# Kernel optimization log

Hardware: AMD Instinct MI355X
Metric: run time of the kernel (lower is better)

Reference implementation:

```python
import jax, jax.numpy as jnp
import numpy as np

N = 50000   # nodes
E = 800000  # edges (avg degree 16)
IN = 3      # in_feats = value(1) + u(2)
H = 128     # hid_feats


def setup_inputs() -> dict:
    key = jax.random.key(0)
    ks = jax.random.split(key, 24)
    value = jax.random.normal(ks[0], (N, 1), jnp.float32)
    u = jax.random.normal(ks[1], (N, 2), jnp.float32)
    src = jax.random.randint(ks[2], (E,), 0, N, dtype=jnp.int32)
    dst = jax.random.randint(ks[3], (E,), 0, N, dtype=jnp.int32)
    dims = [IN, H // 2, H, H, H, H, H, H, H, H, 1]
    inp = {"value": value, "u": u, "src": src, "dst": dst}
    for i in range(10):
        inp[f"W{i+1}"] = jax.random.normal(ks[4 + i], (dims[i], dims[i + 1]), jnp.float32) / np.sqrt(dims[i]).astype(np.float32)
        inp[f"b{i+1}"] = jnp.zeros((dims[i + 1],), jnp.float32)
    return inp


def _gconv(x, src, dst, inv_deg, W, b):
    # DGL GraphConv norm='right': sum incoming src features, divide by in-degree, linear, bias
    agg = jax.ops.segment_sum(x[src], dst, num_segments=N)  # [N, d_in]
    return (agg * inv_deg) @ W + b


def reference(value, u, src, dst, W1, b1, W2, b2, W3, b3, W4, b4, W5, b5,
              W6, b6, W7, b7, W8, b8, W9, b9, W10, b10):
    deg = jax.ops.segment_sum(jnp.ones((E,), jnp.float32), dst, num_segments=N)
    inv_deg = (1.0 / jnp.clip(deg, 1.0))[:, None]  # DGL clamps in-degree to >=1
    lrelu = lambda h: jax.nn.leaky_relu(h, 0.01)
    x = jnp.concatenate([value, u], axis=1)  # [N, 3]
    h = _gconv(x, src, dst, inv_deg, W1, b1)
    h = lrelu(_gconv(h, src, dst, inv_deg, W2, b2))
    h = lrelu(_gconv(h, src, dst, inv_deg, W3, b3))
    h = lrelu(_gconv(h, src, dst, inv_deg, W4, b4))
    h = _gconv(h, src, dst, inv_deg, W5, b5)
    h = _gconv(h, src, dst, inv_deg, W6, b6)
    h = _gconv(h, src, dst, inv_deg, W7, b7)
    h = _gconv(h, src, dst, inv_deg, W8, b8)
    h = jax.nn.sigmoid(_gconv(h, src, dst, inv_deg, W9, b9))
    h = _gconv(h, src, dst, inv_deg, W10, b10)  # [N, 1]
    return h
```

## Files before the change

kernel.cpp:

```cpp
#include <hip/hip_runtime.h>
#include <math.h>

typedef unsigned int u32;
typedef unsigned short u16;
using bf16x8 = __attribute__((ext_vector_type(8))) short;
using f32x4 = __attribute__((ext_vector_type(4))) float;

__device__ inline float bf_lo(u32 v) { return __uint_as_float(v << 16); }
__device__ inline float bf_hi(u32 v) { return __uint_as_float(v & 0xFFFF0000u); }
__device__ inline u16 f2bf(float f) {
    u32 u = __float_as_uint(f);
    return (u16)((u + 0x7FFFu + ((u >> 16) & 1u)) >> 16);
}
__device__ inline float bf2f(u16 h) { return __uint_as_float((u32)h << 16); }
__device__ inline float invdeg(int d) { return 1.0f / (float)(d > 1 ? d : 1); }

#define BIN_SHIFT 13

struct W7 { const float* p[7]; };

__global__ __launch_bounds__(256) void k_front(const int* __restrict__ src,
                                               const int* __restrict__ dst,
                                               int* __restrict__ cur,
                                               u16* __restrict__ colp,
                                               int E, int EB, int SB,
                                               const float* __restrict__ value,
                                               const float* __restrict__ u,
                                               float4* __restrict__ x4, int n, int NBx4,
                                               W7 wp, const float* __restrict__ W64,
                                               u16* __restrict__ hi128, u16* __restrict__ lo128,
                                               u16* __restrict__ hi64, u16* __restrict__ lo64) {
    int blk = blockIdx.x;
    if (blk < SB) {
        const int bin = blk / EB;
        int e = (blk - bin * EB) * 256 + threadIdx.x;
        if (e >= E) return;
        int d = dst[e];
        if ((d >> BIN_SHIFT) != bin) return;
        int slot = atomicAdd(&cur[d], 1);
        if (slot < 64) colp[(size_t)d * 64 + slot] = (u16)src[e];
        return;
    }
    int pb = blk - SB;
    if (pb < NBx4) {
        int i = pb * 256 + threadIdx.x;
        if (i < n) x4[i] = make_float4(value[i], u[2 * i], u[2 * i + 1], 0.f);
        return;
    }
    pb -= NBx4;
    if (pb < 56) {
        const int l = pb >> 3;
        const float* W = wp.p[l];
        int g = (pb & 7) * 256 + threadIdx.x;
        int ct = g >> 8;
        int rem = g & 255;
        int ks = rem >> 6;
        int lane = rem & 63;
        int kbase = ks * 32 + ((lane >> 4) << 3);
        int nn = (ct << 4) + (lane & 15);
        size_t off = ((size_t)l * 2048 + g) * 8;
#pragma unroll
        for (int j = 0; j < 8; ++j) {
            float w = W[(size_t)(kbase + j) * 128 + nn];
            u16 h = f2bf(w);
            hi128[off + j] = h;
            lo128[off + j] = f2bf(w - bf2f(h));
        }
    } else {
        int g = (pb - 56) * 256 + threadIdx.x;
        int ct = g >> 7;
        int rem = g & 127;
        int ks = rem >> 6;
        int lane = rem & 63;
        int kbase = ks * 32 + ((lane >> 4) << 3);
        int nn = (ct << 4) + (lane & 15);
        size_t off = (size_t)g * 8;
#pragma unroll
        for (int j = 0; j < 8; ++j) {
            float w = W64[(size_t)(kbase + j) * 128 + nn];
            u16 h = f2bf(w);
            hi64[off + j] = h;
            lo64[off + j] = f2bf(w - bf2f(h));
        }
    }
}

__global__ __launch_bounds__(256) void k_l1(const float4* __restrict__ x4,
                                            const u16* __restrict__ colp,
                                            const int* __restrict__ deg,
                                            const float* __restrict__ W1,
                                            const float* __restrict__ b1,
                                            u16* __restrict__ out, int nNodes) {
    const int lane = threadIdx.x & 63;
    const int n = blockIdx.x * 4 + (threadIdx.x >> 6);
    if (n >= nNodes) return;
    int dfull = deg[n];
    int dg = dfull > 64 ? 64 : dfull;
    const u16* cl = colp + (size_t)n * 64;
    float a0 = 0.f, a1 = 0.f, a2 = 0.f;
    if (lane < dg) {
        float4 v = x4[cl[lane]];
        a0 = v.x; a1 = v.y; a2 = v.z;
    }
#pragma unroll
    for (int o = 32; o; o >>= 1) {
        a0 += __shfl_xor(a0, o, 64);
        a1 += __shfl_xor(a1, o, 64);
        a2 += __shfl_xor(a2, o, 64);
    }
    float iv = invdeg(dfull);
    float y = b1[lane] + iv * (a0 * W1[lane] + a1 * W1[64 + lane] + a2 * W1[128 + lane]);
    out[(size_t)n * 64 + lane] = f2bf(y);
}

template <int ACT>
__device__ inline float actf(float x) {
    if (ACT == 1) return x > 0.f ? x : 0.01f * x;
    if (ACT == 2) return 1.f / (1.f + expf(-x));
    return x;
}

template <int DIN>
__device__ inline void agg_node(const void* __restrict__ Hin, const u16* __restrict__ colp,
                                const int* __restrict__ deg, u16* __restrict__ aggbuf,
                                int n, int lane) {
    int dfull = deg[n];
    int dg = dfull > 64 ? 64 : dfull;
    const u16* cl = colp + (size_t)n * 64;
    int myc = (lane < dg) ? (int)cl[lane] : 0;
    if (DIN == 128) {
        const u32* H32 = (const u32*)Hin;
        float a0 = 0.f, a1 = 0.f, b0 = 0.f, b1 = 0.f;
        int j = 0;
        for (; j + 8 <= dg; j += 8) {
            u32 v0 = H32[(size_t)__builtin_amdgcn_readlane(myc, j + 0) * 64 + lane];
            u32 v1 = H32[(size_t)__builtin_amdgcn_readlane(myc, j + 1) * 64 + lane];
            u32 v2 = H32[(size_t)__builtin_amdgcn_readlane(myc, j + 2) * 64 + lane];
            u32 v3 = H32[(size_t)__builtin_amdgcn_readlane(myc, j + 3) * 64 + lane];
            u32 v4 = H32[(size_t)__builtin_amdgcn_readlane(myc, j + 4) * 64 + lane];
            u32 v5 = H32[(size_t)__builtin_amdgcn_readlane(myc, j + 5) * 64 + lane];
            u32 v6 = H32[(size_t)__builtin_amdgcn_readlane(myc, j + 6) * 64 + lane];
            u32 v7 = H32[(size_t)__builtin_amdgcn_readlane(myc, j + 7) * 64 + lane];
            a0 += bf_lo(v0) + bf_lo(v1) + bf_lo(v2) + bf_lo(v3);
            a1 += bf_hi(v0) + bf_hi(v1) + bf_hi(v2) + bf_hi(v3);
            b0 += bf_lo(v4) + bf_lo(v5) + bf_lo(v6) + bf_lo(v7);
            b1 += bf_hi(v4) + bf_hi(v5) + bf_hi(v6) + bf_hi(v7);
        }
        for (; j + 4 <= dg; j += 4) {
            u32 v0 = H32[(size_t)__builtin_amdgcn_readlane(myc, j + 0) * 64 + lane];
            u32 v1 = H32[(size_t)__builtin_amdgcn_readlane(myc, j + 1) * 64 + lane];
            u32 v2 = H32[(size_t)__builtin_amdgcn_readlane(myc, j + 2) * 64 + lane];
            u32 v3 = H32[(size_t)__builtin_amdgcn_readlane(myc, j + 3) * 64 + lane];
            a0 += bf_lo(v0) + bf_lo(v1);
            a1 += bf_hi(v0) + bf_hi(v1);
            b0 += bf_lo(v2) + bf_lo(v3);
            b1 += bf_hi(v2) + bf_hi(v3);
        }
        for (; j < dg; ++j) {
            u32 v = H32[(size_t)__builtin_amdgcn_readlane(myc, j) * 64 + lane];
            a0 += bf_lo(v);
            a1 += bf_hi(v);
        }
        float iv = invdeg(dfull);
        ((u32*)aggbuf)[(size_t)n * 64 + lane] =
            (u32)f2bf((a0 + b0) * iv) | ((u32)f2bf((a1 + b1) * iv) << 16);
    } else {
        const u16* H16 = (const u16*)Hin;
        float a0 = 0.f, a1 = 0.f, b0 = 0.f, b1 = 0.f;
        int j = 0;
        for (; j + 8 <= dg; j += 8) {
            u16 v0 = H16[(size_t)__builtin_amdgcn_readlane(myc, j + 0) * 64 + lane];
            u16 v1 = H16[(size_t)__builtin_amdgcn_readlane(myc, j + 1) * 64 + lane];
            u16 v2 = H16[(size_t)__builtin_amdgcn_readlane(myc, j + 2) * 64 + lane];
            u16 v3 = H16[(size_t)__builtin_amdgcn_readlane(myc, j + 3) * 64 + lane];
            u16 v4 = H16[(size_t)__builtin_amdgcn_readlane(myc, j + 4) * 64 + lane];
            u16 v5 = H16[(size_t)__builtin_amdgcn_readlane(myc, j + 5) * 64 + lane];
            u16 v6 = H16[(size_t)__builtin_amdgcn_readlane(myc, j + 6) * 64 + lane];
            u16 v7 = H16[(size_t)__builtin_amdgcn_readlane(myc, j + 7) * 64 + lane];
            a0 += bf2f(v0) + bf2f(v1);
            a1 += bf2f(v2) + bf2f(v3);
            b0 += bf2f(v4) + bf2f(v5);
            b1 += bf2f(v6) + bf2f(v7);
        }
        for (; j + 4 <= dg; j += 4) {
            u16 v0 = H16[(size_t)__builtin_amdgcn_readlane(myc, j + 0) * 64 + lane];
            u16 v1 = H16[(size_t)__builtin_amdgcn_readlane(myc, j + 1) * 64 + lane];
            u16 v2 = H16[(size_t)__builtin_amdgcn_readlane(myc, j + 2) * 64 + lane];
            u16 v3 = H16[(size_t)__builtin_amdgcn_readlane(myc, j + 3) * 64 + lane];
            a0 += bf2f(v0) + bf2f(v1);
            b0 += bf2f(v2) + bf2f(v3);
        }
        for (; j < dg; ++j) {
            a0 += bf2f(H16[(size_t)__builtin_amdgcn_readlane(myc, j) * 64 + lane]);
        }
        aggbuf[(size_t)n * 64 + lane] = f2bf((a0 + a1 + b0 + b1) * invdeg(dfull));
    }
}

template <int DIN, int ACT>
__global__ __launch_bounds__(1024, 8) void k_fuse(const void* __restrict__ Hin,
                                                  const u16* __restrict__ colp,
                                                  const int* __restrict__ deg,
                                                  u16* __restrict__ aggbuf,
                                                  const u16* __restrict__ pkHi,
                                                  const u16* __restrict__ pkLo,
                                                  const float* __restrict__ B,
                                                  u16* __restrict__ Y, int nNodes) {
    const int tid = threadIdx.x;
    const int lane = tid & 63;
    const int w = tid >> 6;
    const int tile = blockIdx.x * 64;

#pragma unroll
    for (int i = 0; i < 4; ++i) {
        int n = tile + w * 4 + i;
        if (n < nNodes) agg_node<DIN>(Hin, colp, deg, aggbuf, n, lane);
    }
    __syncthreads();

    constexpr int NKS = DIN / 32;
    const int m = lane & 15;
    const int kb = lane >> 4;
    const int rg = w & 3;
    const int ct0 = (w >> 2) * 2;
    const int base = tile + rg * 16;
    int arow = base + m;
    if (arow >= nNodes) arow = nNodes - 1;

    bf16x8 aF[NKS];
#pragma unroll
    for (int ks = 0; ks < NKS; ++ks)
        aF[ks] = *reinterpret_cast<const bf16x8*>(aggbuf + (size_t)arow * DIN + ks * 32 + kb * 8);

    const bf16x8* bh = reinterpret_cast<const bf16x8*>(pkHi);
    const bf16x8* bl = reinterpret_cast<const bf16x8*>(pkLo);

#pragma unroll
    for (int c = 0; c < 2; ++c) {
        const int ct = ct0 + c;
        f32x4 acc = {0.f, 0.f, 0.f, 0.f};
#pragma unroll
        for (int ks = 0; ks < NKS; ++ks) {
            acc = __builtin_amdgcn_mfma_f32_16x16x32_bf16(aF[ks], bh[(ct * NKS + ks) * 64 + lane], acc, 0, 0, 0);
            acc = __builtin_amdgcn_mfma_f32_16x16x32_bf16(aF[ks], bl[(ct * NKS + ks) * 64 + lane], acc, 0, 0, 0);
        }
        float bias = B[ct * 16 + m];
#pragma unroll
        for (int r = 0; r < 4; ++r) {
            int row = base + kb * 4 + r;
            if (row < nNodes)
                Y[(size_t)row * 128 + ct * 16 + m] = f2bf(actf<ACT>(acc[r] + bias));
        }
    }
}

__global__ __launch_bounds__(256) void k_agg128b(const u32* __restrict__ H32,
                                                 const u16* __restrict__ colp,
                                                 const int* __restrict__ deg,
                                                 u32* __restrict__ out, int nNodes) {
    const int lane = threadIdx.x & 63;
    const int n = blockIdx.x * 4 + (threadIdx.x >> 6);
    if (n >= nNodes) return;
    agg_node<128>((const void*)H32, colp, deg, (u16*)out, n, lane);
}

__global__ __launch_bounds__(256) void k_mm_last(const u16* __restrict__ A,
                                                 const u16* __restrict__ pkHi,
                                                 const u16* __restrict__ pkLo,
                                                 const float* __restrict__ B,
                                                 const float* __restrict__ w10,
                                                 float* __restrict__ t, int nNodes) {
    const int lane = threadIdx.x & 63;
    const int w = threadIdx.x >> 6;
    const int base = blockIdx.x * 64 + w * 16;
    const int m = lane & 15;
    const int kb = lane >> 4;
    int arow = base + m;
    if (arow >= nNodes) arow = nNodes - 1;

    bf16x8 aF[4];
#pragma unroll
    for (int ks = 0; ks < 4; ++ks)
        aF[ks] = *reinterpret_cast<const bf16x8*>(A + (size_t)arow * 128 + ks * 32 + kb * 8);

    const bf16x8* bh = reinterpret_cast<const bf16x8*>(pkHi);
    const bf16x8* bl = reinterpret_cast<const bf16x8*>(pkLo);

    float p0 = 0.f, p1 = 0.f, p2 = 0.f, p3 = 0.f;
#pragma unroll
    for (int ct = 0; ct < 8; ++ct) {
        f32x4 acc = {0.f, 0.f, 0.f, 0.f};
#pragma unroll
        for (int ks = 0; ks < 4; ++ks) {
            acc = __builtin_amdgcn_mfma_f32_16x16x32_bf16(aF[ks], bh[(ct * 4 + ks) * 64 + lane], acc, 0, 0, 0);
            acc = __builtin_amdgcn_mfma_f32_16x16x32_bf16(aF[ks], bl[(ct * 4 + ks) * 64 + lane], acc, 0, 0, 0);
        }
        float bias = B[ct * 16 + m];
        float wv = w10[ct * 16 + m];
        p0 += wv * actf<2>(acc[0] + bias);
        p1 += wv * actf<2>(acc[1] + bias);
        p2 += wv * actf<2>(acc[2] + bias);
        p3 += wv * actf<2>(acc[3] + bias);
    }
#pragma unroll
    for (int o = 1; o < 16; o <<= 1) {
        p0 += __shfl_xor(p0, o, 64);
        p1 += __shfl_xor(p1, o, 64);
        p2 += __shfl_xor(p2, o, 64);
        p3 += __shfl_xor(p3, o, 64);
    }
    if (m == 0) {
        int r0 = base + kb * 4;
        if (r0 + 0 < nNodes) t[r0 + 0] = p0;
        if (r0 + 1 < nNodes) t[r0 + 1] = p1;
        if (r0 + 2 < nNodes) t[r0 + 2] = p2;
        if (r0 + 3 < nNodes) t[r0 + 3] = p3;
    }
}

__global__ __launch_bounds__(256) void k_aggs(const float* __restrict__ t,
                                              const u16* __restrict__ colp,
                                              const int* __restrict__ deg,
                                              const float* __restrict__ B,
                                              float* __restrict__ out, int nNodes) {
    int n = blockIdx.x * 256 + threadIdx.x;
    if (n >= nNodes) return;
    int dfull = deg[n];
    int dg = dfull > 64 ? 64 : dfull;
    const u16* cl = colp + (size_t)n * 64;
    float s = 0.f;
    for (int j = 0; j < dg; ++j) s += t[cl[j]];
    out[n] = s * invdeg(dfull) + B[0];
}

extern "C" void kernel_launch(void* const* d_in, const int* in_sizes, int n_in,
                              void* d_out, int out_size, void* d_ws, size_t ws_size,
                              hipStream_t stream) {
    const float* value = (const float*)d_in[0];
    const float* u = (const float*)d_in[1];
    const int* src = (const int*)d_in[2];
    const int* dst = (const int*)d_in[3];
    const float* W[10];
    const float* b[10];
    for (int i = 0; i < 10; ++i) {
        W[i] = (const float*)d_in[4 + 2 * i];
        b[i] = (const float*)d_in[5 + 2 * i];
    }
    const int N = in_sizes[0];
    const int E = in_sizes[2];
    float* out = (float*)d_out;

    char* p = (char*)d_ws;
    auto carve = [&](size_t bytes) {
        char* r = p;
        p += (bytes + 255) & ~(size_t)255;
        return r;
    };
    int* deg = (int*)carve((size_t)N * 4);
    u16* colp = (u16*)carve((size_t)N * 64 * 2);
    float4* x4 = (float4*)carve((size_t)N * 16);
    u16* hA = (u16*)carve((size_t)N * 128 * 2);
    u16* hB = (u16*)carve((size_t)N * 128 * 2);
    u16* agg = (u16*)carve((size_t)N * 128 * 2);
    float* t10 = (float*)carve((size_t)N * 4);
    u16* pk128hi = (u16*)carve((size_t)7 * 2048 * 8 * 2);
    u16* pk128lo = (u16*)carve((size_t)7 * 2048 * 8 * 2);
    u16* pk64hi = (u16*)carve((size_t)1024 * 8 * 2);
    u16* pk64lo = (u16*)carve((size_t)1024 * 8 * 2);

    const int nbins = (N + (1 << BIN_SHIFT) - 1) >> BIN_SHIFT;
    const int EB = (E + 255) / 256;
    const int SB = EB * nbins;
    const int NBx4 = (N + 255) / 256;

    hipMemsetAsync(deg, 0, (size_t)N * 4, stream);

    W7 wp;
    for (int i = 0; i < 7; ++i) wp.p[i] = W[2 + i];
    k_front<<<SB + NBx4 + 60, 256, 0, stream>>>(src, dst, deg, colp, E, EB, SB,
                                                value, u, x4, N, NBx4, wp, W[1],
                                                pk128hi, pk128lo, pk64hi, pk64lo);

    const int gw = (N + 3) / 4;
    const int gf = (N + 63) / 64;
    const int gt = (N + 255) / 256;
    const size_t PK = 2048 * 8;

    k_l1<<<gw, 256, 0, stream>>>(x4, colp, deg, W[0], b[0], hA, N);
    k_fuse<64, 1><<<gf, 1024, 0, stream>>>(hA, colp, deg, agg, pk64hi, pk64lo, b[1], hB, N);
    k_fuse<128, 1><<<gf, 1024, 0, stream>>>(hB, colp, deg, agg, pk128hi + 0 * PK, pk128lo + 0 * PK, b[2], hA, N);
    k_fuse<128, 1><<<gf, 1024, 0, stream>>>(hA, colp, deg, agg, pk128hi + 1 * PK, pk128lo + 1 * PK, b[3], hB, N);
    k_fuse<128, 0><<<gf, 1024, 0, stream>>>(hB, colp, deg, agg, pk128hi + 2 * PK, pk128lo + 2 * PK, b[4], hA, N);
    k_fuse<128, 0><<<gf, 1024, 0, stream>>>(hA, colp, deg, agg, pk128hi + 3 * PK, pk128lo + 3 * PK, b[5], hB, N);
    k_fuse<128, 0><<<gf, 1024, 0, stream>>>(hB, colp, deg, agg, pk128hi + 4 * PK, pk128lo + 4 * PK, b[6], hA, N);
    k_fuse<128, 0><<<gf, 1024, 0, stream>>>(hA, colp, deg, agg, pk128hi + 5 * PK, pk128lo + 5 * PK, b[7], hB, N);
    k_agg128b<<<gw, 256, 0, stream>>>((const u32*)hB, colp, deg, (u32*)agg, N);
    k_mm_last<<<gf, 256, 0, stream>>>(agg, pk128hi + 6 * PK, pk128lo + 6 * PK, b[8], W[9], t10, N);
    k_aggs<<<gt, 256, 0, stream>>>(t10, colp, deg, b[9], out, N);
}
```

Baseline: 442.6 us.

## Unfuse aggregation from matmul and gather 16-byte rows with several nodes per wave

Replaces the fused aggregate+MFMA kernels with separate k_aggq and k_mm launches for each layer. The new aggregation kernel gives each lane a 16-byte slice of a row, so one wave handles 4 (DIN=128) or 8 (DIN=64) nodes at once and loads neighbor indices as vectors. The aim is wider, more memory-parallel gathers than the old one-node-per-wave 4-byte loads. In exchange it adds an extra kernel launch and a round trip of the aggregated buffer through global memory per layer. Lanes within a wave also diverge, because the loop runs to the wave-max degree.

Result: faster. 419.0 us (-5.3%).

```diff
diff --git a/kernel.cpp b/kernel.cpp
--- a/kernel.cpp
+++ b/kernel.cpp
@@ -113,6 +113,79 @@
     out[(size_t)n * 64 + lane] = f2bf(y);
 }
 
+template <int DIN>
+__global__ __launch_bounds__(256) void k_aggq(const uint4* __restrict__ H4,
+                                              const u16* __restrict__ colp,
+                                              const int* __restrict__ deg,
+                                              uint4* __restrict__ out, int nNodes) {
+    constexpr int LPN = DIN / 8;
+    constexpr int NPW = 64 / LPN;
+    const int tid = threadIdx.x;
+    const int lane = tid & 63;
+    const int wv = tid >> 6;
+    const int g = lane / LPN;
+    const int c = lane % LPN;
+    const int n = (blockIdx.x * 4 + wv) * NPW + g;
+    const int nn = n < nNodes ? n : nNodes - 1;
+    const int dfull = deg[nn];
+    const int dg = dfull > 64 ? 64 : dfull;
+    const u16* cl = colp + (size_t)nn * 64;
+
+    int dgm = dg;
+#pragma unroll
+    for (int o = 32; o; o >>= 1) {
+        int t = __shfl_xor(dgm, o, 64);
+        dgm = t > dgm ? t : dgm;
+    }
+
+    float acc0 = 0.f, acc1 = 0.f, acc2 = 0.f, acc3 = 0.f;
+    float acc4 = 0.f, acc5 = 0.f, acc6 = 0.f, acc7 = 0.f;
+
+    for (int j = 0; j < dgm; j += 8) {
+        uint4 iv4 = *reinterpret_cast<const uint4*>(cl + j);
+        int s0 = (int)(iv4.x & 0xFFFFu), s1 = (int)(iv4.x >> 16);
+        int s2 = (int)(iv4.y & 0xFFFFu), s3 = (int)(iv4.y >> 16);
+        int s4 = (int)(iv4.z & 0xFFFFu), s5 = (int)(iv4.z >> 16);
+        int s6 = (int)(iv4.w & 0xFFFFu), s7 = (int)(iv4.w >> 16);
+        bool k0 = j + 0 < dg, k1 = j + 1 < dg, k2 = j + 2 < dg, k3 = j + 3 < dg;
+        bool k4 = j + 4 < dg, k5 = j + 5 < dg, k6 = j + 6 < dg, k7 = j + 7 < dg;
+        if (!k0) s0 = 0; if (!k1) s1 = 0; if (!k2) s2 = 0; if (!k3) s3 = 0;
+        if (!k4) s4 = 0; if (!k5) s5 = 0; if (!k6) s6 = 0; if (!k7) s7 = 0;
+        uint4 v0 = H4[(size_t)s0 * LPN + c];
+        uint4 v1 = H4[(size_t)s1 * LPN + c];
+        uint4 v2 = H4[(size_t)s2 * LPN + c];
+        uint4 v3 = H4[(size_t)s3 * LPN + c];
+        uint4 v4 = H4[(size_t)s4 * LPN + c];
+        uint4 v5 = H4[(size_t)s5 * LPN + c];
+        uint4 v6 = H4[(size_t)s6 * LPN + c];
+        uint4 v7 = H4[(size_t)s7 * LPN + c];
+        if (k0) { acc0 += bf_lo(v0.x); acc1 += bf_hi(v0.x); acc2 += bf_lo(v0.y); acc3 += bf_hi(v0.y);
+                  acc4 += bf_lo(v0.z); acc5 += bf_hi(v0.z); acc6 += bf_lo(v0.w); acc7 += bf_hi(v0.w); }
+        if (k1) { acc0 += bf_lo(v1.x); acc1 += bf_hi(v1.x); acc2 += bf_lo(v1.y); acc3 += bf_hi(v1.y);
+                  acc4 += bf_lo(v1.z); acc5 += bf_hi(v1.z); acc6 += bf_lo(v1.w); acc7 += bf_hi(v1.w); }
+        if (k2) { acc0 += bf_lo(v2.x); acc1 += bf_hi(v2.x); acc2 += bf_lo(v2.y); acc3 += bf_hi(v2.y);
+                  acc4 += bf_lo(v2.z); acc5 += bf_hi(v2.z); acc6 += bf_lo(v2.w); acc7 += bf_hi(v2.w); }
+        if (k3) { acc0 += bf_lo(v3.x); acc1 += bf_hi(v3.x); acc2 += bf_lo(v3.y); acc3 += bf_hi(v3.y);
+                  acc4 += bf_lo(v3.z); acc5 += bf_hi(v3.z); acc6 += bf_lo(v3.w); acc7 += bf_hi(v3.w); }
+        if (k4) { acc0 += bf_lo(v4.x); acc1 += bf_hi(v4.x); acc2 += bf_lo(v4.y); acc3 += bf_hi(v4.y);
+                  acc4 += bf_lo(v4.z); acc5 += bf_hi(v4.z); acc6 += bf_lo(v4.w); acc7 += bf_hi(v4.w); }
+        if (k5) { acc0 += bf_lo(v5.x); acc1 += bf_hi(v5.x); acc2 += bf_lo(v5.y); acc3 += bf_hi(v5.y);
+                  acc4 += bf_lo(v5.z); acc5 += bf_hi(v5.z); acc6 += bf_lo(v5.w); acc7 += bf_hi(v5.w); }
+        if (k6) { acc0 += bf_lo(v6.x); acc1 += bf_hi(v6.x); acc2 += bf_lo(v6.y); acc3 += bf_hi(v6.y);
+                  acc4 += bf_lo(v6.z); acc5 += bf_hi(v6.z); acc6 += bf_lo(v6.w); acc7 += bf_hi(v6.w); }
+        if (k7) { acc0 += bf_lo(v7.x); acc1 += bf_hi(v7.x); acc2 += bf_lo(v7.y); acc3 += bf_hi(v7.y);
+                  acc4 += bf_lo(v7.z); acc5 += bf_hi(v7.z); acc6 += bf_lo(v7.w); acc7 += bf_hi(v7.w); }
+    }
+
+    float iv = invdeg(dfull);
+    uint4 o;
+    o.x = (u32)f2bf(acc0 * iv) | ((u32)f2bf(acc1 * iv) << 16);
+    o.y = (u32)f2bf(acc2 * iv) | ((u32)f2bf(acc3 * iv) << 16);
+    o.z = (u32)f2bf(acc4 * iv) | ((u32)f2bf(acc5 * iv) << 16);
+    o.w = (u32)f2bf(acc6 * iv) | ((u32)f2bf(acc7 * iv) << 16);
+    if (n < nNodes) out[(size_t)n * LPN + c] = o;
+}
+
 template <int ACT>
 __device__ inline float actf(float x) {
     if (ACT == 1) return x > 0.f ? x : 0.01f * x;
@@ -120,124 +193,31 @@
     return x;
 }
 
-template <int DIN>
-__device__ inline void agg_node(const void* __restrict__ Hin, const u16* __restrict__ colp,
-                                const int* __restrict__ deg, u16* __restrict__ aggbuf,
-                                int n, int lane) {
-    int dfull = deg[n];
-    int dg = dfull > 64 ? 64 : dfull;
-    const u16* cl = colp + (size_t)n * 64;
-    int myc = (lane < dg) ? (int)cl[lane] : 0;
-    if (DIN == 128) {
-        const u32* H32 = (const u32*)Hin;
-        float a0 = 0.f, a1 = 0.f, b0 = 0.f, b1 = 0.f;
-        int j = 0;
-        for (; j + 8 <= dg; j += 8) {
-            u32 v0 = H32[(size_t)__builtin_amdgcn_readlane(myc, j + 0) * 64 + lane];
-            u32 v1 = H32[(size_t)__builtin_amdgcn_readlane(myc, j + 1) * 64 + lane];
-            u32 v2 = H32[(size_t)__builtin_amdgcn_readlane(myc, j + 2) * 64 + lane];
-            u32 v3 = H32[(size_t)__builtin_amdgcn_readlane(myc, j + 3) * 64 + lane];
-            u32 v4 = H32[(size_t)__builtin_amdgcn_readlane(myc, j + 4) * 64 + lane];
-            u32 v5 = H32[(size_t)__builtin_amdgcn_readlane(myc, j + 5) * 64 + lane];
-            u32 v6 = H32[(size_t)__builtin_amdgcn_readlane(myc, j + 6) * 64 + lane];
-            u32 v7 = H32[(size_t)__builtin_amdgcn_readlane(myc, j + 7) * 64 + lane];
-            a0 += bf_lo(v0) + bf_lo(v1) + bf_lo(v2) + bf_lo(v3);
-            a1 += bf_hi(v0) + bf_hi(v1) + bf_hi(v2) + bf_hi(v3);
-            b0 += bf_lo(v4) + bf_lo(v5) + bf_lo(v6) + bf_lo(v7);
-            b1 += bf_hi(v4) + bf_hi(v5) + bf_hi(v6) + bf_hi(v7);
-        }
-        for (; j + 4 <= dg; j += 4) {
-            u32 v0 = H32[(size_t)__builtin_amdgcn_readlane(myc, j + 0) * 64 + lane];
-            u32 v1 = H32[(size_t)__builtin_amdgcn_readlane(myc, j + 1) * 64 + lane];
-            u32 v2 = H32[(size_t)__builtin_amdgcn_readlane(myc, j + 2) * 64 + lane];
-            u32 v3 = H32[(size_t)__builtin_amdgcn_readlane(myc, j + 3) * 64 + lane];
-            a0 += bf_lo(v0) + bf_lo(v1);
-            a1 += bf_hi(v0) + bf_hi(v1);
-            b0 += bf_lo(v2) + bf_lo(v3);
-            b1 += bf_hi(v2) + bf_hi(v3);
-        }
-        for (; j < dg; ++j) {
-            u32 v = H32[(size_t)__builtin_amdgcn_readlane(myc, j) * 64 + lane];
-            a0 += bf_lo(v);
-            a1 += bf_hi(v);
-        }
-        float iv = invdeg(dfull);
-        ((u32*)aggbuf)[(size_t)n * 64 + lane] =
-            (u32)f2bf((a0 + b0) * iv) | ((u32)f2bf((a1 + b1) * iv) << 16);
-    } else {
-        const u16* H16 = (const u16*)Hin;
-        float a0 = 0.f, a1 = 0.f, b0 = 0.f, b1 = 0.f;
-        int j = 0;
-        for (; j + 8 <= dg; j += 8) {
-            u16 v0 = H16[(size_t)__builtin_amdgcn_readlane(myc, j + 0) * 64 + lane];
-            u16 v1 = H16[(size_t)__builtin_amdgcn_readlane(myc, j + 1) * 64 + lane];
-            u16 v2 = H16[(size_t)__builtin_amdgcn_readlane(myc, j + 2) * 64 + lane];
-            u16 v3 = H16[(size_t)__builtin_amdgcn_readlane(myc, j + 3) * 64 + lane];
-            u16 v4 = H16[(size_t)__builtin_amdgcn_readlane(myc, j + 4) * 64 + lane];
-            u16 v5 = H16[(size_t)__builtin_amdgcn_readlane(myc, j + 5) * 64 + lane];
-            u16 v6 = H16[(size_t)__builtin_amdgcn_readlane(myc, j + 6) * 64 + lane];
-            u16 v7 = H16[(size_t)__builtin_amdgcn_readlane(myc, j + 7) * 64 + lane];
-            a0 += bf2f(v0) + bf2f(v1);
-            a1 += bf2f(v2) + bf2f(v3);
-            b0 += bf2f(v4) + bf2f(v5);
-            b1 += bf2f(v6) + bf2f(v7);
-        }
-        for (; j + 4 <= dg; j += 4) {
-            u16 v0 = H16[(size_t)__builtin_amdgcn_readlane(myc, j + 0) * 64 + lane];
-            u16 v1 = H16[(size_t)__builtin_amdgcn_readlane(myc, j + 1) * 64 + lane];
-            u16 v2 = H16[(size_t)__builtin_amdgcn_readlane(myc, j + 2) * 64 + lane];
-            u16 v3 = H16[(size_t)__builtin_amdgcn_readlane(myc, j + 3) * 64 + lane];
-            a0 += bf2f(v0) + bf2f(v1);
-            b0 += bf2f(v2) + bf2f(v3);
-        }
-        for (; j < dg; ++j) {
-            a0 += bf2f(H16[(size_t)__builtin_amdgcn_readlane(myc, j) * 64 + lane]);
-        }
-        aggbuf[(size_t)n * 64 + lane] = f2bf((a0 + a1 + b0 + b1) * invdeg(dfull));
-    }
-}
-
 template <int DIN, int ACT>
-__global__ __launch_bounds__(1024, 8) void k_fuse(const void* __restrict__ Hin,
-                                                  const u16* __restrict__ colp,
-                                                  const int* __restrict__ deg,
-                                                  u16* __restrict__ aggbuf,
-                                                  const u16* __restrict__ pkHi,
-                                                  const u16* __restrict__ pkLo,
-                                                  const float* __restrict__ B,
-                                                  u16* __restrict__ Y, int nNodes) {
-    const int tid = threadIdx.x;
-    const int lane = tid & 63;
-    const int w = tid >> 6;
-    const int tile = blockIdx.x * 64;
-
-#pragma unroll
-    for (int i = 0; i < 4; ++i) {
-        int n = tile + w * 4 + i;
-        if (n < nNodes) agg_node<DIN>(Hin, colp, deg, aggbuf, n, lane);
-    }
-    __syncthreads();
-
+__global__ __launch_bounds__(256) void k_mm(const u16* __restrict__ A,
+                                            const u16* __restrict__ pkHi,
+                                            const u16* __restrict__ pkLo,
+                                            const float* __restrict__ B,
+                                            u16* __restrict__ Y, int nNodes) {
     constexpr int NKS = DIN / 32;
+    const int lane = threadIdx.x & 63;
+    const int w = threadIdx.x >> 6;
+    const int base = blockIdx.x * 64 + w * 16;
     const int m = lane & 15;
     const int kb = lane >> 4;
-    const int rg = w & 3;
-    const int ct0 = (w >> 2) * 2;
-    const int base = tile + rg * 16;
     int arow = base + m;
     if (arow >= nNodes) arow = nNodes - 1;
 
     bf16x8 aF[NKS];
 #pragma unroll
     for (int ks = 0; ks < NKS; ++ks)
-        aF[ks] = *reinterpret_cast<const bf16x8*>(aggbuf + (size_t)arow * DIN + ks * 32 + kb * 8);
+        aF[ks] = *reinterpret_cast<const bf16x8*>(A + (size_t)arow * DIN + ks * 32 + kb * 8);
 
     const bf16x8* bh = reinterpret_cast<const bf16x8*>(pkHi);
     const bf16x8* bl = reinterpret_cast<const bf16x8*>(pkLo);
 
 #pragma unroll
-    for (int c = 0; c < 2; ++c) {
-        const int ct = ct0 + c;
+    for (int ct = 0; ct < 8; ++ct) {
         f32x4 acc = {0.f, 0.f, 0.f, 0.f};
 #pragma unroll
         for (int ks = 0; ks < NKS; ++ks) {
@@ -252,16 +232,6 @@
                 Y[(size_t)row * 128 + ct * 16 + m] = f2bf(actf<ACT>(acc[r] + bias));
         }
     }
-}
-
-__global__ __launch_bounds__(256) void k_agg128b(const u32* __restrict__ H32,
-                                                 const u16* __restrict__ colp,
-                                                 const int* __restrict__ deg,
-                                                 u32* __restrict__ out, int nNodes) {
-    const int lane = threadIdx.x & 63;
-    const int n = blockIdx.x * 4 + (threadIdx.x >> 6);
-    if (n >= nNodes) return;
-    agg_node<128>((const void*)H32, colp, deg, (u16*)out, n, lane);
 }
 
 __global__ __launch_bounds__(256) void k_mm_last(const u16* __restrict__ A,
@@ -382,19 +352,28 @@
                                                 pk128hi, pk128lo, pk64hi, pk64lo);
 
     const int gw = (N + 3) / 4;
-    const int gf = (N + 63) / 64;
+    const int gq128 = (N + 15) / 16;
+    const int gq64 = (N + 31) / 32;
+    const int gg = (N + 63) / 64;
     const int gt = (N + 255) / 256;
     const size_t PK = 2048 * 8;
 
     k_l1<<<gw, 256, 0, stream>>>(x4, colp, deg, W[0], b[0], hA, N);
-    k_fuse<64, 1><<<gf, 1024, 0, stream>>>(hA, colp, deg, agg, pk64hi, pk64lo, b[1], hB, N);
-    k_fuse<128, 1><<<gf, 1024, 0, stream>>>(hB, colp, deg, agg, pk128hi + 0 * PK, pk128lo + 0 * PK, b[2], hA, N);
-    k_fuse<128, 1><<<gf, 1024, 0, stream>>>(hA, colp, deg, agg, pk128hi + 1 * PK, pk128lo + 1 * PK, b[3], hB, N);
-    k_fuse<128, 0><<<gf, 1024, 0, stream>>>(hB, colp, deg, agg, pk128hi + 2 * PK, pk128lo + 2 * PK, b[4], hA, N);
-    k_fuse<128, 0><<<gf, 1024, 0, stream>>>(hA, colp, deg, agg, pk128hi + 3 * PK, pk128lo + 3 * PK, b[5], hB, N);
-    k_fuse<128, 0><<<gf, 1024, 0, stream>>>(hB, colp, deg, agg, pk128hi + 4 * PK, pk128lo + 4 * PK, b[6], hA, N);
-    k_fuse<128, 0><<<gf, 1024, 0, stream>>>(hA, colp, deg, agg, pk128hi + 5 * PK, pk128lo + 5 * PK, b[7], hB, N);
-    k_agg128b<<<gw, 256, 0, stream>>>((const u32*)hB, colp, deg, (u32*)agg, N);
-    k_mm_last<<<gf, 256, 0, stream>>>(agg, pk128hi + 6 * PK, pk128lo + 6 * PK, b[8], W[9], t10, N);
+    k_aggq<64><<<gq64, 256, 0, stream>>>((const uint4*)hA, colp, deg, (uint4*)agg, N);
+    k_mm<64, 1><<<gg, 256, 0, stream>>>(agg, pk64hi, pk64lo, b[1], hB, N);
+    k_aggq<128><<<gq128, 256, 0, stream>>>((const uint4*)hB, colp, deg, (uint4*)agg, N);
+    k_mm<128, 1><<<gg, 256, 0, stream>>>(agg, pk128hi + 0 * PK, pk128lo + 0 * PK, b[2], hA, N);
+    k_aggq<128><<<gq128, 256, 0, stream>>>((const uint4*)hA, colp, deg, (uint4*)agg, N);
+    k_mm<128, 1><<<gg, 256, 0, stream>>>(agg, pk128hi + 1 * PK, pk128lo + 1 * PK, b[3], hB, N);
+    k_aggq<128><<<gq128, 256, 0, stream>>>((const uint4*)hB, colp, deg, (uint4*)agg, N);
+    k_mm<128, 0><<<gg, 256, 0, stream>>>(agg, pk128hi + 2 * PK, pk128lo + 2 * PK, b[4], hA, N);
+    k_aggq<128><<<gq128, 256, 0, stream>>>((const uint4*)hA, colp, deg, (uint4*)agg, N);
+    k_mm<128, 0><<<gg, 256, 0, stream>>>(agg, pk128hi + 3 * PK, pk128lo + 3 * PK, b[5], hB, N);
+    k_aggq<128><<<gq128, 256, 0, stream>>>((const uint4*)hB, colp, deg, (uint4*)agg, N);
+    k_mm<128, 0><<<gg, 256, 0, stream>>>(agg, pk128hi + 4 * PK, pk128lo + 4 * PK, b[6], hA, N);
+    k_aggq<128><<<gq128, 256, 0, stream>>>((const uint4*)hA, colp, deg, (uint4*)agg, N);
+    k_mm<128, 0><<<gg, 256, 0, stream>>>(agg, pk128hi + 5 * PK, pk128lo + 5 * PK, b[7], hB, N);
+    k_aggq<128><<<gq128, 256, 0, stream>>>((const uint4*)hB, colp, deg, (uint4*)agg, N);
+    k_mm_last<<<gg, 256, 0, stream>>>(agg, pk128hi + 6 * PK, pk128lo + 6 * PK, b[8], W[9], t10, N);
     k_aggs<<<gt, 256, 0, stream>>>(t10, colp, deg, b[9], out, N);
 }
```
